# Kernel tuning notes

Hardware: AMD Instinct MI355X
Metric: run time of the kernel (lower is better)

## Reference

```python
import jax, jax.numpy as jnp
import numpy as np

BN_EPS = 1e-5

def _bn_relu(x, gamma, beta):
    # BatchNorm1d in training mode: batch stats over (B, N) per channel
    mean = jnp.mean(x, axis=(0, 1), keepdims=True)
    var = jnp.var(x, axis=(0, 1), keepdims=True)
    return jax.nn.relu((x - mean) * jax.lax.rsqrt(var + BN_EPS) * gamma + beta)

def setup_inputs() -> dict:
    key = jax.random.key(0)
    ks = jax.random.split(key, 8)
    B, N, S, C1, C2 = 8, 8192, 2048, 128, 256
    return {
        'xyz1': jax.random.normal(ks[0], (B, N, 3), jnp.float32),
        'xyz2': jax.random.normal(ks[1], (B, S, 3), jnp.float32),
        'points1': jax.random.normal(ks[2], (B, N, C1), jnp.float32),
        'points2': jax.random.normal(ks[3], (B, S, C2), jnp.float32),
        'w0': jax.random.normal(ks[4], (256, C1 + C2), jnp.float32) * 0.02,
        'b0': jnp.zeros((256,), jnp.float32),
        'g0': jnp.ones((256,), jnp.float32),
        'be0': jnp.zeros((256,), jnp.float32),
        'w1': jax.random.normal(ks[5], (128, 256), jnp.float32) * 0.02,
        'b1': jnp.zeros((128,), jnp.float32),
        'g1': jnp.ones((128,), jnp.float32),
        'be1': jnp.zeros((128,), jnp.float32),
    }

def reference(xyz1, xyz2, points1, points2, w0, b0, g0, be0, w1, b1, g1, be1):
    # squared pairwise distances [B, N, S]
    sq = (jnp.sum(xyz1 * xyz1, -1)[:, :, None]
          - 2.0 * jnp.einsum('bnc,bmc->bnm', xyz1, xyz2)
          + jnp.sum(xyz2 * xyz2, -1)[:, None, :])
    neg_d, idx = jax.lax.top_k(-sq, 3)          # smallest 3 distances
    dist = -neg_d                               # [B, N, 3]
    recip = 1.0 / (dist + 1e-8)
    weight = recip / jnp.sum(recip, -1, keepdims=True)
    gathered = jax.vmap(lambda p, i: p[i])(points2, idx)   # [B, N, 3, C2]
    interp = jnp.sum(gathered * weight[..., None], axis=2)  # [B, N, C2]
    x = jnp.concatenate([points1, interp], axis=-1)         # [B, N, C1+C2]
    x = _bn_relu(jnp.einsum('bnc,oc->bno', x, w0) + b0, g0, be0)
    x = _bn_relu(jnp.einsum('bnc,oc->bno', x, w1) + b1, g1, be1)
    return x
```

## Files before the change

kernel.cpp:

```cpp
#include <hip/hip_runtime.h>

#define B_  8
#define N_  8192
#define S_  2048
#define C1_ 128
#define C2_ 256
#define KA_ 384
#define H0_ 256
#define H1_ 128
#define R_  (B_ * N_)

typedef __bf16 bf16;
typedef __attribute__((ext_vector_type(2))) __bf16 bf16x2;
typedef __attribute__((ext_vector_type(4))) __bf16 bf16x4;
typedef __attribute__((ext_vector_type(8))) __bf16 bf16x8;
typedef __attribute__((ext_vector_type(4))) float f32x4;

__device__ __forceinline__ void gload_lds16(const void* g, void* l) {
    __builtin_amdgcn_global_load_lds(
        (const __attribute__((address_space(1))) void*)g,
        (__attribute__((address_space(3))) void*)l, 16, 0, 0);
}

__global__ __launch_bounds__(256) void prep_kernel(const float* __restrict__ w0,
                                                   const float* __restrict__ w1,
                                                   bf16* __restrict__ Wbf0,
                                                   bf16* __restrict__ Wbf1,
                                                   float* __restrict__ stats)
{
    int blk = blockIdx.x, tid = threadIdx.x;
    if (blk < 96) {
        int i = blk * 256 + tid;
        float4 v = *(const float4*)(w0 + (size_t)i * 4);
        bf16x4 o = { (bf16)v.x, (bf16)v.y, (bf16)v.z, (bf16)v.w };
        *(bf16x4*)(Wbf0 + (size_t)i * 4) = o;
    } else if (blk < 128) {
        int i = (blk - 96) * 256 + tid;
        float4 v = *(const float4*)(w1 + (size_t)i * 4);
        bf16x4 o = { (bf16)v.x, (bf16)v.y, (bf16)v.z, (bf16)v.w };
        *(bf16x4*)(Wbf1 + (size_t)i * 4) = o;
    } else {
        #pragma unroll
        for (int k = 0; k < 3; ++k) stats[k * 256 + tid] = 0.f;
    }
}

__global__ __launch_bounds__(256) void top3_interp_kernel(
    const float* __restrict__ xyz1, const float* __restrict__ xyz2,
    const float* __restrict__ points1, const float* __restrict__ points2,
    bf16* __restrict__ Abf)
{
    __shared__ float4 sc[S_];
    __shared__ float  md[64][4][3];
    __shared__ int    mi[64][4][3];
    __shared__ int    sidx[64][3];
    __shared__ float  sw[64][3];

    int b = blockIdx.x >> 7;
    int ntile = blockIdx.x & 127;
    const float* src = xyz2 + (size_t)b * S_ * 3;
    for (int i = threadIdx.x; i < S_; i += 256) {
        float x = src[i * 3 + 0], y = src[i * 3 + 1], z = src[i * 3 + 2];
        float4 c; c.x = x; c.y = y; c.z = z; c.w = x * x + y * y + z * z;
        sc[i] = c;
    }
    __syncthreads();

    const int q  = threadIdx.x >> 2;
    const int sp = threadIdx.x & 3;
    const size_t row = (size_t)b * N_ + ntile * 64 + q;
    const float ax = -2.f * xyz1[row * 3 + 0];
    const float ay = -2.f * xyz1[row * 3 + 1];
    const float az = -2.f * xyz1[row * 3 + 2];

    float m0 = 1e30f, m1 = 1e30f, m2 = 1e30f;
    int   j0 = 0, j1 = 0, j2 = 0;

    #pragma unroll 4
    for (int i = 0; i < S_ / 4; ++i) {
        int s = i * 4 + sp;
        float4 c = sc[s];
        float m = fmaf(ax, c.x, fmaf(ay, c.y, fmaf(az, c.z, c.w)));
        if (m < m2) {
            if (m < m1) {
                m2 = m1; j2 = j1;
                if (m < m0) { m1 = m0; j1 = j0; m0 = m; j0 = s; }
                else        { m1 = m;  j1 = s; }
            } else { m2 = m; j2 = s; }
        }
    }
    md[q][sp][0] = m0; md[q][sp][1] = m1; md[q][sp][2] = m2;
    mi[q][sp][0] = j0; mi[q][sp][1] = j1; mi[q][sp][2] = j2;
    __syncthreads();

    if (threadIdx.x < 64) {
        int qq = threadIdx.x;
        float d0 = md[qq][0][0], d1 = md[qq][0][1], d2 = md[qq][0][2];
        int   i0 = mi[qq][0][0], i1 = mi[qq][0][1], i2 = mi[qq][0][2];
        #pragma unroll
        for (int p = 1; p < 4; ++p) {
            #pragma unroll
            for (int j = 0; j < 3; ++j) {
                float d = md[qq][p][j]; int s = mi[qq][p][j];
                bool lt2 = (d < d2) || (d == d2 && s < i2);
                if (lt2) {
                    bool lt1 = (d < d1) || (d == d1 && s < i1);
                    if (lt1) {
                        d2 = d1; i2 = i1;
                        bool lt0 = (d < d0) || (d == d0 && s < i0);
                        if (lt0) { d1 = d0; i1 = i0; d0 = d; i0 = s; }
                        else     { d1 = d;  i1 = s; }
                    } else { d2 = d; i2 = s; }
                }
            }
        }
        size_t orow = (size_t)b * N_ + ntile * 64 + qq;
        float px = xyz1[orow * 3 + 0], py = xyz1[orow * 3 + 1], pz = xyz1[orow * 3 + 2];
        float pp = px * px + py * py + pz * pz;
        float r0 = 1.f / (d0 + pp + 1e-8f);
        float r1 = 1.f / (d1 + pp + 1e-8f);
        float r2 = 1.f / (d2 + pp + 1e-8f);
        float inv = 1.f / (r0 + r1 + r2);
        sidx[qq][0] = i0; sidx[qq][1] = i1; sidx[qq][2] = i2;
        sw[qq][0] = r0 * inv; sw[qq][1] = r1 * inv; sw[qq][2] = r2 * inv;
    }
    __syncthreads();

    const int wv = threadIdx.x >> 6, ln = threadIdx.x & 63;
    const size_t rowbase = (size_t)b * N_ + ntile * 64;
    const float* p2 = points2 + (size_t)b * S_ * C2_;
    for (int r = wv; r < 64; r += 4) {
        size_t orow = rowbase + r;
        int ia = sidx[r][0], ib = sidx[r][1], ic = sidx[r][2];
        float wa = sw[r][0], wb = sw[r][1], wc = sw[r][2];
        float4 va = *(const float4*)(p2 + (size_t)ia * C2_ + ln * 4);
        float4 vb = *(const float4*)(p2 + (size_t)ib * C2_ + ln * 4);
        float4 vc = *(const float4*)(p2 + (size_t)ic * C2_ + ln * 4);
        bf16x4 o = { (bf16)(wa * va.x + wb * vb.x + wc * vc.x),
                     (bf16)(wa * va.y + wb * vb.y + wc * vc.y),
                     (bf16)(wa * va.z + wb * vb.z + wc * vc.z),
                     (bf16)(wa * va.w + wb * vb.w + wc * vc.w) };
        *(bf16x4*)(Abf + orow * KA_ + C1_ + ln * 4) = o;

        float2 p = *(const float2*)(points1 + orow * C1_ + ln * 2);
        bf16x2 po = { (bf16)p.x, (bf16)p.y };
        *(bf16x2*)(Abf + orow * KA_ + ln * 2) = po;
    }
}

template<int K, int OT, bool OUTBF>
__global__ __launch_bounds__(256) void mfma_gemm_kernel(
    const bf16* __restrict__ A, const bf16* __restrict__ Wt, void* __restrict__ Cout,
    float* __restrict__ sums, float* __restrict__ sumsq)
{
    __shared__ bf16 As[128 * 32];
    __shared__ bf16 Bs[128 * 32];
    __shared__ float csum[128], csumsq[128];
    const int tid = threadIdx.x;
    const int lane = tid & 63, wave = tid >> 6;
    const int wr = wave >> 1, wc = wave & 1;
    const int r0 = blockIdx.x * 128, o0 = blockIdx.y * 128;

    f32x4 acc[4][4] = {};

    const int l15 = lane & 15, g = lane >> 4;
    const int slot = g ^ ((l15 >> 1) & 3);
    int a_off[4], b_off[4];
    #pragma unroll
    for (int m = 0; m < 4; ++m) a_off[m] = (wr * 64 + m * 16 + l15) * 32 + slot * 8;
    #pragma unroll
    for (int n = 0; n < 4; ++n) b_off[n] = (wc * 64 + n * 16 + l15) * 32 + slot * 8;

    const int c0 = tid, c1 = tid + 256;
    const int ar0 = c0 >> 2, ar1 = c1 >> 2;
    const int kb0 = ((c0 & 3) ^ ((ar0 >> 1) & 3)) * 8;
    const int kb1 = ((c1 & 3) ^ ((ar1 >> 1) & 3)) * 8;

    if (tid < 128) { csum[tid] = 0.f; csumsq[tid] = 0.f; }

    for (int k0 = 0; k0 < K; k0 += 32) {
        __syncthreads();
        gload_lds16(A  + (size_t)(r0 + ar0) * K + k0 + kb0, &As[c0 * 8]);
        gload_lds16(A  + (size_t)(r0 + ar1) * K + k0 + kb1, &As[c1 * 8]);
        gload_lds16(Wt + (size_t)(o0 + ar0) * K + k0 + kb0, &Bs[c0 * 8]);
        gload_lds16(Wt + (size_t)(o0 + ar1) * K + k0 + kb1, &Bs[c1 * 8]);
        __syncthreads();
        bf16x8 af[4], bfr[4];
        #pragma unroll
        for (int m = 0; m < 4; ++m) af[m]  = *(const bf16x8*)&As[a_off[m]];
        #pragma unroll
        for (int n = 0; n < 4; ++n) bfr[n] = *(const bf16x8*)&Bs[b_off[n]];
        #pragma unroll
        for (int m = 0; m < 4; ++m)
            #pragma unroll
            for (int n = 0; n < 4; ++n)
                acc[m][n] = __builtin_amdgcn_mfma_f32_16x16x32_bf16(af[m], bfr[n], acc[m][n], 0, 0, 0);
    }

    const int crow = r0 + wr * 64 + g * 4;
    const int ccol = o0 + wc * 64 + l15;
    #pragma unroll
    for (int m = 0; m < 4; ++m)
        #pragma unroll
        for (int n = 0; n < 4; ++n)
            #pragma unroll
            for (int j = 0; j < 4; ++j) {
                size_t off = (size_t)(crow + m * 16 + j) * OT + ccol + n * 16;
                if (OUTBF) ((bf16*)Cout)[off] = (bf16)acc[m][n][j];
                else       ((float*)Cout)[off] = acc[m][n][j];
            }

    #pragma unroll
    for (int n = 0; n < 4; ++n) {
        float s = 0.f, q = 0.f;
        #pragma unroll
        for (int m = 0; m < 4; ++m)
            #pragma unroll
            for (int j = 0; j < 4; ++j) {
                float v = acc[m][n][j];
                s += v; q = fmaf(v, v, q);
            }
        int col = wc * 64 + n * 16 + l15;
        atomicAdd(&csum[col], s);
        atomicAdd(&csumsq[col], q);
    }
    __syncthreads();
    if (tid < 128) {
        atomicAdd(&sums[o0 + tid], csum[tid]);
        atomicAdd(&sumsq[o0 + tid], csumsq[tid]);
    }
}

__global__ __launch_bounds__(256) void mfma_gemm2_kernel(
    const bf16* __restrict__ Ahp, const bf16* __restrict__ Wt,
    const float* __restrict__ sums0, const float* __restrict__ sumsq0,
    const float* __restrict__ g0, const float* __restrict__ be0,
    float* __restrict__ Cout, float* __restrict__ sums, float* __restrict__ sumsq)
{
    constexpr int K = H0_, OT = H1_;
    __shared__ bf16 As[128 * 32];
    __shared__ bf16 Bs[128 * 32];
    __shared__ float csum[128], csumsq[128];
    __shared__ float sscale[256], sshift[256];
    const int tid = threadIdx.x;
    const int lane = tid & 63, wave = tid >> 6;
    const int wr = wave >> 1, wc = wave & 1;
    const int r0 = blockIdx.x * 128, o0 = blockIdx.y * 128;

    {
        const float invR = 1.f / (float)R_;
        float mean = sums0[tid] * invR;
        float var = sumsq0[tid] * invR - mean * mean;
        float sv = g0[tid] * rsqrtf(var + 1e-5f);
        sscale[tid] = sv;
        sshift[tid] = be0[tid] - mean * sv;
    }
    if (tid < 128) { csum[tid] = 0.f; csumsq[tid] = 0.f; }
    __syncthreads();

    f32x4 acc[4][4] = {};

    const int l15 = lane & 15, g = lane >> 4;
    const int slot = g ^ ((l15 >> 1) & 3);
    int a_off[4], b_off[4];
    #pragma unroll
    for (int m = 0; m < 4; ++m) a_off[m] = (wr * 64 + m * 16 + l15) * 32 + slot * 8;
    #pragma unroll
    for (int n = 0; n < 4; ++n) b_off[n] = (wc * 64 + n * 16 + l15) * 32 + slot * 8;

    const int c0 = tid, c1 = tid + 256;
    const int ar0 = c0 >> 2, ar1 = c1 >> 2;
    const int kb0 = ((c0 & 3) ^ ((ar0 >> 1) & 3)) * 8;
    const int kb1 = ((c1 & 3) ^ ((ar1 >> 1) & 3)) * 8;

    for (int k0 = 0; k0 < K; k0 += 32) {
        bf16x8 va0 = *(const bf16x8*)(Ahp + (size_t)(r0 + ar0) * K + k0 + kb0);
        bf16x8 va1 = *(const bf16x8*)(Ahp + (size_t)(r0 + ar1) * K + k0 + kb1);
        float s0a[8], h0a[8], s1a[8], h1a[8];
        *(float4*)&s0a[0] = *(const float4*)(&sscale[k0 + kb0]);
        *(float4*)&s0a[4] = *(const float4*)(&sscale[k0 + kb0 + 4]);
        *(float4*)&h0a[0] = *(const float4*)(&sshift[k0 + kb0]);
        *(float4*)&h0a[4] = *(const float4*)(&sshift[k0 + kb0 + 4]);
        *(float4*)&s1a[0] = *(const float4*)(&sscale[k0 + kb1]);
        *(float4*)&s1a[4] = *(const float4*)(&sscale[k0 + kb1 + 4]);
        *(float4*)&h1a[0] = *(const float4*)(&sshift[k0 + kb1]);
        *(float4*)&h1a[4] = *(const float4*)(&sshift[k0 + kb1 + 4]);
        bf16x8 ra0, ra1;
        #pragma unroll
        for (int j = 0; j < 8; ++j) {
            float f0 = fmaxf(0.f, fmaf((float)va0[j], s0a[j], h0a[j]));
            float f1 = fmaxf(0.f, fmaf((float)va1[j], s1a[j], h1a[j]));
            ra0[j] = (bf16)f0; ra1[j] = (bf16)f1;
        }
        __syncthreads();
        gload_lds16(Wt + (size_t)(o0 + ar0) * K + k0 + kb0, &Bs[c0 * 8]);
        gload_lds16(Wt + (size_t)(o0 + ar1) * K + k0 + kb1, &Bs[c1 * 8]);
        *(bf16x8*)&As[c0 * 8] = ra0;
        *(bf16x8*)&As[c1 * 8] = ra1;
        __syncthreads();
        bf16x8 af[4], bfr[4];
        #pragma unroll
        for (int m = 0; m < 4; ++m) af[m]  = *(const bf16x8*)&As[a_off[m]];
        #pragma unroll
        for (int n = 0; n < 4; ++n) bfr[n] = *(const bf16x8*)&Bs[b_off[n]];
        #pragma unroll
        for (int m = 0; m < 4; ++m)
            #pragma unroll
            for (int n = 0; n < 4; ++n)
                acc[m][n] = __builtin_amdgcn_mfma_f32_16x16x32_bf16(af[m], bfr[n], acc[m][n], 0, 0, 0);
    }

    const int crow = r0 + wr * 64 + g * 4;
    const int ccol = o0 + wc * 64 + l15;
    #pragma unroll
    for (int m = 0; m < 4; ++m)
        #pragma unroll
        for (int n = 0; n < 4; ++n)
            #pragma unroll
            for (int j = 0; j < 4; ++j)
                ((float*)Cout)[(size_t)(crow + m * 16 + j) * OT + ccol + n * 16] = acc[m][n][j];

    #pragma unroll
    for (int n = 0; n < 4; ++n) {
        float s = 0.f, q = 0.f;
        #pragma unroll
        for (int m = 0; m < 4; ++m)
            #pragma unroll
            for (int j = 0; j < 4; ++j) {
                float v = acc[m][n][j];
                s += v; q = fmaf(v, v, q);
            }
        int col = wc * 64 + n * 16 + l15;
        atomicAdd(&csum[col], s);
        atomicAdd(&csumsq[col], q);
    }
    __syncthreads();
    if (tid < 128) {
        atomicAdd(&sums[o0 + tid], csum[tid]);
        atomicAdd(&sumsq[o0 + tid], csumsq[tid]);
    }
}

__global__ __launch_bounds__(256) void bnrelu_kernel(
    float* __restrict__ X, const float* __restrict__ sums1,
    const float* __restrict__ sumsq1, const float* __restrict__ g1,
    const float* __restrict__ be1)
{
    __shared__ float ss[128], sh[128];
    int tid = threadIdx.x;
    if (tid < 128) {
        const float invR = 1.f / (float)R_;
        float mean = sums1[tid] * invR;
        float var = sumsq1[tid] * invR - mean * mean;
        float sv = g1[tid] * rsqrtf(var + 1e-5f);
        ss[tid] = sv;
        sh[tid] = be1[tid] - mean * sv;
    }
    __syncthreads();

    #pragma unroll
    for (int it = 0; it < 4; ++it) {
        size_t i = (size_t)it * 524288 + (size_t)blockIdx.x * 256 + tid;
        int c = ((int)i & 31) * 4;
        float4 v = *(float4*)(X + i * 4);
        v.x = fmaxf(0.f, v.x * ss[c + 0] + sh[c + 0]);
        v.y = fmaxf(0.f, v.y * ss[c + 1] + sh[c + 1]);
        v.z = fmaxf(0.f, v.z * ss[c + 2] + sh[c + 2]);
        v.w = fmaxf(0.f, v.w * ss[c + 3] + sh[c + 3]);
        *(float4*)(X + i * 4) = v;
    }
}

extern "C" void kernel_launch(void* const* d_in, const int* in_sizes, int n_in,
                              void* d_out, int out_size, void* d_ws, size_t ws_size,
                              hipStream_t stream)
{
    const float* xyz1    = (const float*)d_in[0];
    const float* xyz2    = (const float*)d_in[1];
    const float* points1 = (const float*)d_in[2];
    const float* points2 = (const float*)d_in[3];
    const float* w0  = (const float*)d_in[4];
    const float* g0  = (const float*)d_in[6];
    const float* be0 = (const float*)d_in[7];
    const float* w1  = (const float*)d_in[8];
    const float* g1  = (const float*)d_in[10];
    const float* be1 = (const float*)d_in[11];
    float* out = (float*)d_out;
    char* ws = (char*)d_ws;

    bf16* Abf     = (bf16*)(ws);
    bf16* hpre_bf = (bf16*)(ws + 50331648);
    bf16* Wbf0    = (bf16*)(ws + 117440512);
    bf16* Wbf1    = (bf16*)(ws + 117637120);
    float* stats  = (float*)(ws + 119275520);
    float* sums0 = stats,        *sumsq0 = stats + 256;
    float* sums1 = stats + 512,  *sumsq1 = stats + 640;

    prep_kernel<<<129, 256, 0, stream>>>(w0, w1, Wbf0, Wbf1, stats);
    top3_interp_kernel<<<B_ * (N_ / 64), 256, 0, stream>>>(xyz1, xyz2, points1, points2, Abf);

    mfma_gemm_kernel<KA_, H0_, true><<<dim3(R_ / 128, 2), 256, 0, stream>>>(
        Abf, Wbf0, hpre_bf, sums0, sumsq0);

    mfma_gemm2_kernel<<<dim3(R_ / 128, 1), 256, 0, stream>>>(
        hpre_bf, Wbf1, sums0, sumsq0, g0, be0, out, sums1, sumsq1);

    bnrelu_kernel<<<2048, 256, 0, stream>>>(out, sums1, sumsq1, g1, be1);
}
```

Baseline: 175.0 us.

## Precompute xyz2 float4 candidates in prep kernel and read them from global

Moves the per-block construction of the padded xyz2 candidate array (coords plus squared norm) out of the top-3 kernel and into the prep kernel, writing it once to a global workspace buffer. The top-3 loop now reads candidates directly from global or cache instead of LDS, dropping the LDS fill and its barrier. A block-index swizzle spreads neighbouring blocks across batches. The risk is that per-thread global float4 loads in the hot inner loop have more latency than LDS reads, and the swizzle may hurt L2 locality for the per-batch candidate set.

```diff
diff --git a/kernel.cpp b/kernel.cpp
--- a/kernel.cpp
+++ b/kernel.cpp
@@ -24,9 +24,11 @@
 
 __global__ __launch_bounds__(256) void prep_kernel(const float* __restrict__ w0,
                                                    const float* __restrict__ w1,
+                                                   const float* __restrict__ xyz2,
                                                    bf16* __restrict__ Wbf0,
                                                    bf16* __restrict__ Wbf1,
-                                                   float* __restrict__ stats)
+                                                   float* __restrict__ stats,
+                                                   float4* __restrict__ c4g)
 {
     int blk = blockIdx.x, tid = threadIdx.x;
     if (blk < 96) {
@@ -39,32 +41,34 @@
         float4 v = *(const float4*)(w1 + (size_t)i * 4);
         bf16x4 o = { (bf16)v.x, (bf16)v.y, (bf16)v.z, (bf16)v.w };
         *(bf16x4*)(Wbf1 + (size_t)i * 4) = o;
+    } else if (blk == 128) {
+        #pragma unroll
+        for (int k = 0; k < 3; ++k) stats[k * 256 + tid] = 0.f;
     } else {
-        #pragma unroll
-        for (int k = 0; k < 3; ++k) stats[k * 256 + tid] = 0.f;
+        int i = (blk - 129) * 256 + tid;
+        float x = xyz2[(size_t)i * 3 + 0];
+        float y = xyz2[(size_t)i * 3 + 1];
+        float z = xyz2[(size_t)i * 3 + 2];
+        float4 c; c.x = x; c.y = y; c.z = z; c.w = x * x + y * y + z * z;
+        c4g[i] = c;
     }
 }
 
 __global__ __launch_bounds__(256) void top3_interp_kernel(
-    const float* __restrict__ xyz1, const float* __restrict__ xyz2,
+    const float* __restrict__ xyz1, const float4* __restrict__ c4g,
     const float* __restrict__ points1, const float* __restrict__ points2,
     bf16* __restrict__ Abf)
 {
-    __shared__ float4 sc[S_];
     __shared__ float  md[64][4][3];
     __shared__ int    mi[64][4][3];
     __shared__ int    sidx[64][3];
     __shared__ float  sw[64][3];
 
-    int b = blockIdx.x >> 7;
-    int ntile = blockIdx.x & 127;
-    const float* src = xyz2 + (size_t)b * S_ * 3;
-    for (int i = threadIdx.x; i < S_; i += 256) {
-        float x = src[i * 3 + 0], y = src[i * 3 + 1], z = src[i * 3 + 2];
-        float4 c; c.x = x; c.y = y; c.z = z; c.w = x * x + y * y + z * z;
-        sc[i] = c;
-    }
-    __syncthreads();
+    int swz = (blockIdx.x & 7) * 128 + (blockIdx.x >> 3);
+    int b = swz >> 7;
+    int ntile = swz & 127;
+
+    const float4* cand = c4g + (size_t)b * S_;
 
     const int q  = threadIdx.x >> 2;
     const int sp = threadIdx.x & 3;
@@ -79,7 +83,7 @@
     #pragma unroll 4
     for (int i = 0; i < S_ / 4; ++i) {
         int s = i * 4 + sp;
-        float4 c = sc[s];
+        float4 c = cand[s];
         float m = fmaf(ax, c.x, fmaf(ay, c.y, fmaf(az, c.z, c.w)));
         if (m < m2) {
             if (m < m1) {
@@ -393,11 +397,12 @@
     bf16* Wbf0    = (bf16*)(ws + 117440512);
     bf16* Wbf1    = (bf16*)(ws + 117637120);
     float* stats  = (float*)(ws + 119275520);
+    float4* c4g   = (float4*)(ws + 119279616);
     float* sums0 = stats,        *sumsq0 = stats + 256;
     float* sums1 = stats + 512,  *sumsq1 = stats + 640;
 
-    prep_kernel<<<129, 256, 0, stream>>>(w0, w1, Wbf0, Wbf1, stats);
-    top3_interp_kernel<<<B_ * (N_ / 64), 256, 0, stream>>>(xyz1, xyz2, points1, points2, Abf);
+    prep_kernel<<<193, 256, 0, stream>>>(w0, w1, xyz2, Wbf0, Wbf1, stats, c4g);
+    top3_interp_kernel<<<B_ * (N_ / 64), 256, 0, stream>>>(xyz1, c4g, points1, points2, Abf);
 
     mfma_gemm_kernel<KA_, H0_, true><<<dim3(R_ / 128, 2), 256, 0, stream>>>(
         Abf, Wbf0, hpre_bf, sums0, sumsq0);
```

Measured after the change: 218.2 us. 24.7% more time.
